# Kernel optimization log

Measured on AMD Instinct MI355X. Metric: run time of the kernel, lower is better.

Reference implementation:

```python
import jax, jax.numpy as jnp
import numpy as np

N = 50000      # num nodes
E = 400000     # directed edges (avg out-degree 8)
DIN = 128
DOUT = 128
ALPHA = 0.5    # args.alphaDir (buffer, requires_grad=False)
BETA = 0.5     # args.betaDir
GAMA = 0.5     # args.gamaDir


def _dedupe(rows, cols, vals, n):
    key = rows.astype(np.int64) * n + cols.astype(np.int64)
    uk, inv = np.unique(key, return_inverse=True)
    v = np.bincount(inv, weights=vals, minlength=uk.shape[0])
    return (uk // n).astype(np.int32), (uk % n).astype(np.int32), v.astype(np.float32)


def _dir_norm(r, c, v, n):
    # directed_norm: D_out^{-1/2} A D_in^{-1/2}, inf -> 0
    in_deg = np.bincount(c, weights=v, minlength=n)
    out_deg = np.bincount(r, weights=v, minlength=n)
    in_is = np.zeros(n); m = in_deg > 0; in_is[m] = in_deg[m] ** -0.5
    out_is = np.zeros(n); m = out_deg > 0; out_is[m] = out_deg[m] ** -0.5
    return r, c, (out_is[r] * v * in_is[c]).astype(np.float32)


def _spgemm(rA, cA, vA, rB, cB, vB, n):
    # sparse @ sparse in COO, vectorized numpy
    order = np.argsort(rB, kind='stable')
    rBs, cBs, vBs = rB[order], cB[order], vB[order]
    degB = np.bincount(rBs, minlength=n)
    indptr = np.concatenate(([0], np.cumsum(degB)))
    counts = degB[cA]
    total = int(counts.sum())
    rep = np.repeat(np.arange(len(rA)), counts)
    first = np.cumsum(counts) - counts
    pos = np.arange(total) - np.repeat(first, counts) + np.repeat(indptr[cA], counts)
    rows = rA[rep]
    cols = cBs[pos]
    vals = vA[rep].astype(np.float64) * vBs[pos]
    return _dedupe(rows, cols, vals, n)


def setup_inputs() -> dict:
    rng = np.random.default_rng(0)
    r0 = rng.integers(0, N, E).astype(np.int64)
    c0 = rng.integers(0, N, E).astype(np.int64)
    r, c, v = _dedupe(r0, c0, np.ones(E, np.float32), N)
    a = _dir_norm(r, c, v, N)                 # adj_norm
    at = _dir_norm(c, r, v, N)                # adj_t_norm
    rr, cc, vv = _spgemm(a[0], a[1], a[2], at[0], at[1], at[2], N)
    aat = _dir_norm(rr, cc, vv, N)            # directed_norm(A @ At)
    rr, cc, vv = _spgemm(at[0], at[1], at[2], a[0], a[1], a[2], N)
    ata = _dir_norm(rr, cc, vv, N)            # directed_norm(At @ A)
    rr, cc, vv = _spgemm(a[0], a[1], a[2], a[0], a[1], a[2], N)
    aa = _dir_norm(rr, cc, vv, N)             # directed_norm(A @ A)
    rr, cc, vv = _spgemm(at[0], at[1], at[2], at[0], at[1], at[2], N)
    atat = _dir_norm(rr, cc, vv, N)           # directed_norm(At @ At)

    key = jax.random.key(0)
    ks = jax.random.split(key, 7)
    x = jax.random.normal(ks[0], (N, DIN), dtype=jnp.float32)
    s = 1.0 / np.sqrt(DIN)

    def lin(k):
        k1, k2 = jax.random.split(k)
        w = jax.random.uniform(k1, (DIN, DOUT), jnp.float32, -s, s)
        b = jax.random.uniform(k2, (DOUT,), jnp.float32, -s, s)
        return w, b

    w_sd, b_sd = lin(ks[1]); w_ds, b_ds = lin(ks[2])
    w0, b0 = lin(ks[3]); w1, b1 = lin(ks[4])
    w2, b2 = lin(ks[5]); w3, b3 = lin(ks[6])

    out = {'x': x,
           'w_sd': w_sd, 'b_sd': b_sd, 'w_ds': w_ds, 'b_ds': b_ds,
           'w0': w0, 'b0': b0, 'w1': w1, 'b1': b1,
           'w2': w2, 'b2': b2, 'w3': w3, 'b3': b3}
    for name, t in (('a', a), ('at', at), ('aat', aat), ('ata', ata), ('aa', aa), ('atat', atat)):
        out[name + '_rows'] = jnp.asarray(t[0])
        out[name + '_cols'] = jnp.asarray(t[1])
        out[name + '_vals'] = jnp.asarray(t[2])
    return out


def _spmm(rows, cols, vals, x):
    # (A @ x)[i] = sum_e vals[e] * x[cols[e]] scattered to rows[e]
    return jax.ops.segment_sum(vals[:, None] * x[cols], rows, num_segments=x.shape[0])


def reference(x, a_rows, a_cols, a_vals, at_rows, at_cols, at_vals,
              aat_rows, aat_cols, aat_vals, ata_rows, ata_cols, ata_vals,
              aa_rows, aa_cols, aa_vals, atat_rows, atat_cols, atat_vals,
              w_sd, b_sd, w_ds, b_ds, w0, b0, w1, b1, w2, b2, w3, b3):
    out1 = ALPHA * (_spmm(a_rows, a_cols, a_vals, x) @ w_sd + b_sd) \
         + (1.0 - ALPHA) * (_spmm(at_rows, at_cols, at_vals, x) @ w_ds + b_ds)
    out2 = BETA * (_spmm(aat_rows, aat_cols, aat_vals, x) @ w0 + b0) \
         + (1.0 - BETA) * (_spmm(ata_rows, ata_cols, ata_vals, x) @ w1 + b1)
    out3 = GAMA * (_spmm(aa_rows, aa_cols, aa_vals, x) @ w2 + b2) \
         + (1.0 - GAMA) * (_spmm(atat_rows, atat_cols, atat_vals, x) @ w3 + b3)
    return out1 + out2 + out3
```

## Files before the change

### kernel.cpp

```cpp
#include <hip/hip_runtime.h>
#include <hip/hip_bf16.h>

#define FD 128

typedef __attribute__((ext_vector_type(8))) short bf16x8;
typedef __attribute__((ext_vector_type(4))) float f32x4;

__device__ __forceinline__ float bfu2f(unsigned short u) {
  return __uint_as_float(((unsigned int)u) << 16);
}
__device__ __forceinline__ float b2f(__hip_bfloat16 v) { return __bfloat162float(v); }
__device__ __forceinline__ unsigned int pk2(float lo, float hi) {
  return (unsigned int)__bfloat16_as_ushort(__float2bfloat16(lo)) |
         ((unsigned int)__bfloat16_as_ushort(__float2bfloat16(hi)) << 16);
}

__device__ __forceinline__ float ldf(const void* p, int i, int ff) {
  return ff ? ((const float*)p)[i] : b2f(((const __hip_bfloat16*)p)[i]);
}
__device__ __forceinline__ int ldi(const void* p, int i, int fi) {
  return fi ? (int)((const long long*)p)[i] : ((const int*)p)[i];
}

__global__ void cvtall_k(const void* __restrict__ rows, const void* __restrict__ cols,
                         const void* __restrict__ vals, int nnz, int n,
                         const void* __restrict__ x,
                         int* __restrict__ r32, int* __restrict__ c32,
                         float* __restrict__ vf, int* __restrict__ cntT,
                         int* flags) {
  __shared__ int cnt[2];
  if (threadIdx.x < 2) cnt[threadIdx.x] = 0;
  __syncthreads();
  const unsigned short* xu = (const unsigned short*)x;
  int big = 0;
  for (int i = threadIdx.x; i < 1024; i += 256) {
    int e = (xu[i] >> 7) & 0xFF;
    if (e >= 0x90) big++;
  }
  if (big) atomicAdd(&cnt[0], big);
  const int* ci = (const int*)cols;
  int zeros = 0;
  for (int i = threadIdx.x; i < 128; i += 256)
    if ((i & 1) && ci[i] == 0) zeros++;
  if (zeros) atomicAdd(&cnt[1], zeros);
  __syncthreads();
  int ff = (cnt[0] > 16) ? 1 : 0;
  int fi = (cnt[1] >= 32) ? 1 : 0;
  if (blockIdx.x == 0 && threadIdx.x == 0) {
    flags[0] = ff;
    flags[1] = fi;
  }
  int i = blockIdx.x * 256 + threadIdx.x;
  if (i >= nnz) return;
  int r = ldi(rows, i, fi);
  int c = ldi(cols, i, fi);
  if ((unsigned)r >= (unsigned)n) r = 0;
  if ((unsigned)c >= (unsigned)n) c = 0;
  r32[i] = r;
  c32[i] = c;
  vf[i] = ldf(vals, i, ff);
  atomicAdd(&cntT[c], 1);
}

__global__ void scanAbs_k(const int* __restrict__ cnt, int n, int* bsum,
                          const int* __restrict__ rows, int nnz, int* rpA, int nb) {
  int blk = blockIdx.x;
  if (blk < nb) {
    __shared__ int sh[256];
    int t = threadIdx.x;
    int i = blk * 256 + t;
    sh[t] = (i < n) ? cnt[i] : 0;
    __syncthreads();
    for (int d = 128; d > 0; d >>= 1) {
      if (t < d) sh[t] += sh[t + d];
      __syncthreads();
    }
    if (t == 0) bsum[blk] = sh[0];
  } else {
    int i = (blk - nb) * 256 + threadIdx.x;
    if (i > n) return;
    int lo = 0, hi = nnz;
    while (lo < hi) { int mid = (lo + hi) >> 1; if (rows[mid] < i) lo = mid + 1; else hi = mid; }
    rpA[i] = lo;
  }
}

__global__ void scanB_k(int* bsum, int nb, int* rpTail) {
  __shared__ int sh[256];
  int t = threadIdx.x;
  int v = (t < nb) ? bsum[t] : 0;
  sh[t] = v;
  __syncthreads();
  int val = v;
  for (int d = 1; d < 256; d <<= 1) {
    int add = (t >= d) ? sh[t - d] : 0;
    __syncthreads();
    val += add;
    sh[t] = val;
    __syncthreads();
  }
  if (t < nb) bsum[t] = val - v;
  if (t == 255) *rpTail = val;
}

__global__ void scanC_k(const int* __restrict__ cnt, int n, const int* __restrict__ bsum,
                        int* rp, int* cur) {
  __shared__ int sh[256];
  int t = threadIdx.x;
  int i = blockIdx.x * 256 + t;
  int v = (i < n) ? cnt[i] : 0;
  sh[t] = v;
  __syncthreads();
  int val = v;
  for (int d = 1; d < 256; d <<= 1) {
    int add = (t >= d) ? sh[t - d] : 0;
    __syncthreads();
    val += add;
    sh[t] = val;
    __syncthreads();
  }
  int ex = val - v + bsum[blockIdx.x];
  if (i < n) { rp[i] = ex; cur[i] = ex; }
}

__global__ void scatter_k(const int* __restrict__ r, const int* __restrict__ c,
                          const float* __restrict__ v, int nnz,
                          int* cur, int* tSrc, float* tVal) {
  int i = blockIdx.x * 256 + threadIdx.x;
  if (i >= nnz) return;
  int p = atomicAdd(&cur[c[i]], 1);
  if ((unsigned)p >= (unsigned)nnz) return;
  tSrc[p] = r[i];
  tVal[p] = v[i];
}

__global__ void nodesum_k(const int* __restrict__ rpA, const float* __restrict__ av,
                          const int* __restrict__ rpT, const float* __restrict__ tv,
                          float* __restrict__ u1, float* __restrict__ v1, int n) {
  int i = blockIdx.x * 256 + threadIdx.x;
  if (i >= n) return;
  float su = 0.f;
  int e0 = rpA[i], e1 = rpA[i + 1];
  for (int j = e0; j < e1; ++j) su += av[j];
  u1[i] = su;
  float sv = 0.f;
  int f0 = rpT[i], f1 = rpT[i + 1];
  for (int j = f0; j < f1; ++j) sv += tv[j];
  v1[i] = sv;
}

__global__ void bias_k(const void* a, const void* b, const void* c, const void* d,
                       const void* e, const void* f, float* bias, const int* flags) {
  int ff = flags[0];
  int i = threadIdx.x;
  bias[i] = 0.5f * (ldf(a, i, ff) + ldf(b, i, ff) + ldf(c, i, ff)
                  + ldf(d, i, ff) + ldf(e, i, ff) + ldf(f, i, ff));
}

__global__ void fill_k(unsigned short* o, int n) {
  int i = blockIdx.x * 256 + threadIdx.x;
  if (i < n) o[i] = 0x3E80;
}

struct W6p { const void* w[6]; };
struct B6p { const void* b[6]; };

__global__ void dpp_k(const int* __restrict__ rpA, const int* __restrict__ ci,
                      const float* __restrict__ av,
                      const int* __restrict__ rpT, const int* __restrict__ ti,
                      const float* __restrict__ tv,
                      const float* __restrict__ u1, const float* __restrict__ v1,
                      float* __restrict__ s1, float* __restrict__ s2,
                      float* __restrict__ s3, float* __restrict__ s4, int n,
                      const void* __restrict__ x, unsigned int* __restrict__ xb, int nx,
                      W6p ws, __hip_bfloat16* __restrict__ Wt,
                      B6p bs, float* __restrict__ bias,
                      const int* flags, int nb, int cvtB) {
  int blk = blockIdx.x;
  if (blk < nb) {
    int i = blk * 256 + threadIdx.x;
    if (i >= n) return;
    float a1 = 0.f, a3 = 0.f;
    int s0 = rpA[i], se = rpA[i + 1];
    for (int j = s0; j < se; ++j) {
      int c = ci[j];
      float v = av[j];
      a1 = fmaf(v, v1[c], a1);
      a3 = fmaf(v, u1[c], a3);
    }
    s1[i] = (a1 > 0.f) ? rsqrtf(a1) : 0.f;
    s3[i] = (a3 > 0.f) ? rsqrtf(a3) : 0.f;
    float a2 = 0.f, a4 = 0.f;
    int t0 = rpT[i], t1 = rpT[i + 1];
    for (int j = t0; j < t1; ++j) {
      int r = ti[j];
      float v = tv[j];
      a2 = fmaf(v, u1[r], a2);
      a4 = fmaf(v, v1[r], a4);
    }
    s2[i] = (a2 > 0.f) ? rsqrtf(a2) : 0.f;
    s4[i] = (a4 > 0.f) ? rsqrtf(a4) : 0.f;
    return;
  }
  int ff = flags[0];
  if (blk < nb + cvtB) {
    int i = ((blk - nb) * 256 + threadIdx.x) * 8;
    if (i >= nx) return;
    uint4 o;
    if (ff) {
      float4 p0 = *(const float4*)((const float*)x + i);
      float4 p1 = *(const float4*)((const float*)x + i + 4);
      o.x = pk2(p0.x, p0.y); o.y = pk2(p0.z, p0.w);
      o.z = pk2(p1.x, p1.y); o.w = pk2(p1.z, p1.w);
    } else {
      o = *(const uint4*)((const unsigned short*)x + i);
    }
    *(uint4*)(xb + i / 2) = o;
    return;
  }
  if (blk < nb + cvtB + 384) {
    int e = (blk - nb - cvtB) * 256 + threadIdx.x;
    if (e >= 6 * 16384) return;
    int seg = e >> 14;
    int r = e & 16383;
    int nn = r >> 7;
    int innerB = (r & 127) << 1;
    int kb = innerB ^ ((nn & 7) << 4);
    int k = kb >> 1;
    Wt[e] = __float2bfloat16(ldf(ws.w[seg], k * 128 + nn, ff));
    return;
  }
  int i = threadIdx.x;
  if (i < FD)
    bias[i] = 0.5f * (ldf(bs.b[0], i, ff) + ldf(bs.b[1], i, ff) + ldf(bs.b[2], i, ff)
                    + ldf(bs.b[3], i, ff) + ldf(bs.b[4], i, ff) + ldf(bs.b[5], i, ff));
}

__global__ void epk_k(const int* __restrict__ cA, const float* __restrict__ vA,
                      const float* __restrict__ sA1, const float* __restrict__ sA2,
                      const int* __restrict__ cT, const float* __restrict__ vT,
                      const float* __restrict__ sT1, const float* __restrict__ sT2,
                      float4* __restrict__ ewA, float4* __restrict__ ewT, int nnz) {
  int i = blockIdx.x * 256 + threadIdx.x;
  if (i < nnz) {
    int c = cA[i];
    float v = vA[i];
    ewA[i] = make_float4(v, v * sA1[c], v * sA2[c], 0.f);
  } else if (i < 2 * nnz) {
    int k = i - nnz;
    int c = cT[k];
    float v = vT[k];
    ewT[k] = make_float4(v, v * sT1[c], v * sT2[c], 0.f);
  }
}

struct FHSet {
  const int* rp; const int* ci; const float4* ew;
  unsigned int* ot; unsigned int* oa; unsigned int* ob;
};

__global__ __launch_bounds__(256) void fh3d_k(
    FHSet h0, FHSet h1, const unsigned int* __restrict__ xb, int n, int half) {
  int blk = blockIdx.x;
  bool hiH = blk >= half;
  const int* rp = hiH ? h1.rp : h0.rp;
  const int* ci = hiH ? h1.ci : h0.ci;
  const float4* ew = hiH ? h1.ew : h0.ew;
  unsigned int* ot = hiH ? h1.ot : h0.ot;
  unsigned int* oa = hiH ? h1.oa : h0.oa;
  unsigned int* ob = hiH ? h1.ob : h0.ob;
  int bb = hiH ? blk - half : blk;

  int wave = threadIdx.x >> 6;
  int l = threadIdx.x & 63;
  int r = bb * 4 + wave;
  if (r >= n) return;
  int s = rp[r], e = rp[r + 1];

  float tl = 0.f, th = 0.f, al = 0.f, ah = 0.f, bl = 0.f, bh = 0.f;
  int j = s;
  for (; j + 3 < e; j += 4) {
#pragma unroll
    for (int u = 0; u < 4; ++u) {
      int c = ci[j + u];
      float4 w = ew[j + u];
      unsigned int xu = xb[(size_t)c * 64 + l];
      float lo = __uint_as_float(xu << 16);
      float hi = __uint_as_float(xu & 0xFFFF0000u);
      tl = fmaf(w.x, lo, tl); th = fmaf(w.x, hi, th);
      al = fmaf(w.y, lo, al); ah = fmaf(w.y, hi, ah);
      bl = fmaf(w.z, lo, bl); bh = fmaf(w.z, hi, bh);
    }
  }
  for (; j < e; ++j) {
    int c = ci[j];
    float4 w = ew[j];
    unsigned int xu = xb[(size_t)c * 64 + l];
    float lo = __uint_as_float(xu << 16);
    float hi = __uint_as_float(xu & 0xFFFF0000u);
    tl = fmaf(w.x, lo, tl); th = fmaf(w.x, hi, th);
    al = fmaf(w.y, lo, al); ah = fmaf(w.y, hi, ah);
    bl = fmaf(w.z, lo, bl); bh = fmaf(w.z, hi, bh);
  }
  ot[(size_t)r * 64 + l] = pk2(tl, th);
  oa[(size_t)r * 128 + l] = pk2(al, ah);
  ob[(size_t)r * 128 + l] = pk2(bl, bh);
}

struct SHSet {
  const int* rp; const int* ci; const float* cv;
  const unsigned int* gp;
  unsigned int* ya; unsigned int* yb;
  const float* rsa; const float* rsb;
};

__global__ __launch_bounds__(256) void sh2d_k(SHSet h0, SHSet h1, int n, int half) {
  int blk = blockIdx.x;
  bool hiH = blk >= half;
  const int* rp = hiH ? h1.rp : h0.rp;
  const int* ci = hiH ? h1.ci : h0.ci;
  const float* cv = hiH ? h1.cv : h0.cv;
  const unsigned int* gp = hiH ? h1.gp : h0.gp;
  unsigned int* ya = hiH ? h1.ya : h0.ya;
  unsigned int* yb = hiH ? h1.yb : h0.yb;
  const float* rsa = hiH ? h1.rsa : h0.rsa;
  const float* rsb = hiH ? h1.rsb : h0.rsb;
  int bb = hiH ? blk - half : blk;

  int wave = threadIdx.x >> 6;
  int l = threadIdx.x & 63;
  int lf = l & 31;
  bool hlo = l < 32;
  int r = bb * 4 + wave;
  if (r >= n) return;
  int s = rp[r], e = rp[r + 1];

  float f0 = 0.f, f1 = 0.f, f2 = 0.f, f3 = 0.f;
  int j = s;
  for (; j + 3 < e; j += 4) {
#pragma unroll
    for (int u = 0; u < 4; ++u) {
      int c = ci[j + u];
      float v = cv[j + u];
      uint2 g = *(const uint2*)(gp + (size_t)c * 128 + l * 2);
      f0 = fmaf(v, __uint_as_float(g.x << 16), f0);
      f1 = fmaf(v, __uint_as_float(g.x & 0xFFFF0000u), f1);
      f2 = fmaf(v, __uint_as_float(g.y << 16), f2);
      f3 = fmaf(v, __uint_as_float(g.y & 0xFFFF0000u), f3);
    }
  }
  for (; j < e; ++j) {
    int c = ci[j];
    float v = cv[j];
    uint2 g = *(const uint2*)(gp + (size_t)c * 128 + l * 2);
    f0 = fmaf(v, __uint_as_float(g.x << 16), f0);
    f1 = fmaf(v, __uint_as_float(g.x & 0xFFFF0000u), f1);
    f2 = fmaf(v, __uint_as_float(g.y << 16), f2);
    f3 = fmaf(v, __uint_as_float(g.y & 0xFFFF0000u), f3);
  }
  float rs = hlo ? rsa[r] : rsb[r];
  unsigned int* yp = hlo ? ya : yb;
  uint2 o;
  o.x = pk2(f0 * rs, f1 * rs);
  o.y = pk2(f2 * rs, f3 * rs);
  *(uint2*)(yp + (size_t)r * 64 + lf * 2) = o;
}

struct Y6 { const unsigned short* y[6]; };

__global__ __launch_bounds__(256) void gemm6m3_k(
    Y6 ys, const unsigned short* __restrict__ Wt2, const float* __restrict__ bias,
    void* __restrict__ outp, int M, const int* flags) {
  int ff = flags[0];
  __shared__ __align__(16) unsigned short Bs[16384];
  const int tid = threadIdx.x;
  const int lane = tid & 63;
  const int wave = tid >> 6;
  const int m = lane & 15;
  const int q = lane >> 4;
  const int r0 = blockIdx.x * 128 + wave * 32;
  const int row0 = r0 + m;
  const int row1 = r0 + 16 + m;
  const bool ok0 = row0 < M;
  const bool ok1 = row1 < M;
  const bf16x8 zero8 = {0, 0, 0, 0, 0, 0, 0, 0};

  f32x4 acc0[8], acc1[8];
#pragma unroll
  for (int nt = 0; nt < 8; ++nt) {
    acc0[nt] = (f32x4){0.f, 0.f, 0.f, 0.f};
    acc1[nt] = (f32x4){0.f, 0.f, 0.f, 0.f};
  }

  bf16x8 Bst[8];
#pragma unroll
  for (int c2 = 0; c2 < 8; ++c2)
    Bst[c2] = *(const bf16x8*)(Wt2 + (size_t)(c2 * 256 + tid) * 8);
  bf16x8 Ap0[4], Ap1[4];
#pragma unroll
  for (int kc = 0; kc < 4; ++kc) {
    Ap0[kc] = ok0 ? *(const bf16x8*)(ys.y[0] + (size_t)row0 * FD + kc * 32 + q * 8) : zero8;
    Ap1[kc] = ok1 ? *(const bf16x8*)(ys.y[0] + (size_t)row1 * FD + kc * 32 + q * 8) : zero8;
  }

  const int swz = (m & 7) << 4;

#pragma unroll
  for (int t = 0; t < 6; ++t) {
    __syncthreads();
#pragma unroll
    for (int c2 = 0; c2 < 8; ++c2)
      *(bf16x8*)((char*)Bs + (size_t)(c2 * 256 + tid) * 16) = Bst[c2];
    bf16x8 A0[4], A1[4];
#pragma unroll
    for (int kc = 0; kc < 4; ++kc) { A0[kc] = Ap0[kc]; A1[kc] = Ap1[kc]; }
    if (t < 5) {
#pragma unroll
      for (int c2 = 0; c2 < 8; ++c2)
        Bst[c2] = *(const bf16x8*)(Wt2 + (size_t)(t + 1) * 16384 +
                                   (size_t)(c2 * 256 + tid) * 8);
#pragma unroll
      for (int kc = 0; kc < 4; ++kc) {
        Ap0[kc] = ok0 ? *(const bf16x8*)(ys.y[t + 1] + (size_t)row0 * FD + kc * 32 + q * 8) : zero8;
        Ap1[kc] = ok1 ? *(const bf16x8*)(ys.y[t + 1] + (size_t)row1 * FD + kc * 32 + q * 8) : zero8;
      }
    }
    __syncthreads();
#pragma unroll
    for (int kc = 0; kc < 4; ++kc) {
      const int koff = (kc * 64 + q * 16) ^ swz;
#pragma unroll
      for (int nt = 0; nt < 8; ++nt) {
        const int nrow = nt * 16 + m;
        bf16x8 bfv = *(const bf16x8*)((const char*)Bs + nrow * 256 + koff);
        acc0[nt] = __builtin_amdgcn_mfma_f32_16x16x32_bf16(A0[kc], bfv, acc0[nt], 0, 0, 0);
        acc1[nt] = __builtin_amdgcn_mfma_f32_16x16x32_bf16(A1[kc], bfv, acc1[nt], 0, 0, 0);
      }
    }
  }

#pragma unroll
  for (int nt = 0; nt < 8; ++nt) {
    int col = nt * 16 + m;
    float bv = bias[col];
#pragma unroll
    for (int rg = 0; rg < 4; ++rg) {
      int g0 = r0 + q * 4 + rg;
      if (g0 < M) {
        float v = 0.5f * acc0[nt][rg] + bv;
        if (ff) ((float*)outp)[(size_t)g0 * FD + col] = v;
        else ((unsigned short*)outp)[(size_t)g0 * FD + col] =
            __bfloat16_as_ushort(__float2bfloat16(v));
      }
      int g1 = r0 + 16 + q * 4 + rg;
      if (g1 < M) {
        float v = 0.5f * acc1[nt][rg] + bv;
        if (ff) ((float*)outp)[(size_t)g1 * FD + col] = v;
        else ((unsigned short*)outp)[(size_t)g1 * FD + col] =
            __bfloat16_as_ushort(__float2bfloat16(v));
      }
    }
  }
}

__global__ __launch_bounds__(128) void spmm_k(
    const int* __restrict__ rp, const void* __restrict__ ci, int cif,
    const void* __restrict__ cv, int cvf,
    const void* __restrict__ x, int xf, __hip_bfloat16* __restrict__ y,
    int n, int nnzMax,
    const float* __restrict__ cscale, const float* __restrict__ rscale,
    const int* flags) {
  int ff = flags[0], fi = flags[1];
  int vf = cvf ? 1 : ff;
  int iw = cif ? fi : 0;
  int xw = xf ? ff : 0;
  const int t = threadIdx.x;
  int r0 = blockIdx.x * 4;
  int rend = min(r0 + 4, n);
  for (int r = r0; r < rend; ++r) {
    int s = rp[r], e = rp[r + 1];
    s = max(0, min(s, nnzMax));
    e = max(s, min(e, nnzMax));
    float acc = 0.f;
    for (int j = s; j < e; ++j) {
      int c = ldi(ci, j, iw);
      if ((unsigned)c >= (unsigned)n) c = 0;
      float v = (vf ? ((const float*)cv)[j] : b2f(((const __hip_bfloat16*)cv)[j]));
      if (cscale) v *= cscale[c];
      float xv = xw ? ((const float*)x)[c * FD + t]
                    : b2f(((const __hip_bfloat16*)x)[c * FD + t]);
      acc = fmaf(v, xv, acc);
    }
    if (rscale) acc *= rscale[r];
    y[r * FD + t] = __float2bfloat16(acc);
  }
}

__global__ __launch_bounds__(256) void gemm_k(
    const __hip_bfloat16* __restrict__ Y, const void* __restrict__ W,
    const float* __restrict__ bias, const void* __restrict__ accin,
    void* __restrict__ outp, int M, const int* flags) {
  int ff = flags[0];
  __shared__ __align__(16) float Wl[32 * 128];
  __shared__ __align__(16) float Yl[64 * 36];
  const int t = threadIdx.x;
  const int row0 = blockIdx.x * 64;
  const int c4 = (t & 31) * 4;
  const int r8 = (t >> 5) * 8;
  const int rs = t >> 3;
  const int q = t & 7;
  float acc[8][4];
#pragma unroll
  for (int m = 0; m < 8; ++m)
#pragma unroll
    for (int j = 0; j < 4; ++j) acc[m][j] = 0.f;
  for (int kc = 0; kc < 4; ++kc) {
    if (ff) {
      const float4* Wg4 = (const float4*)((const float*)W + kc * 32 * 128);
#pragma unroll
      for (int i = 0; i < 4; ++i)
        *(float4*)(Wl + (t + i * 256) * 4) = Wg4[t + i * 256];
    } else {
      const ushort4* Wg4 = (const ushort4*)((const unsigned short*)W + kc * 32 * 128);
#pragma unroll
      for (int i = 0; i < 4; ++i) {
        ushort4 u = Wg4[t + i * 256];
        int base = (t + i * 256) * 4;
        Wl[base + 0] = bfu2f(u.x);
        Wl[base + 1] = bfu2f(u.y);
        Wl[base + 2] = bfu2f(u.z);
        Wl[base + 3] = bfu2f(u.w);
      }
    }
#pragma unroll
    for (int i = 0; i < 2; ++i) {
      int rr = rs + i * 32;
      int grow = row0 + rr;
      ushort4 u = make_ushort4(0, 0, 0, 0);
      if (grow < M)
        u = *(const ushort4*)((const unsigned short*)Y + grow * FD + kc * 32 + q * 4);
      float* yd = Yl + rr * 36 + q * 4;
      yd[0] = bfu2f(u.x); yd[1] = bfu2f(u.y); yd[2] = bfu2f(u.z); yd[3] = bfu2f(u.w);
    }
    __syncthreads();
#pragma unroll
    for (int kk = 0; kk < 32; kk += 4) {
      float4 w0 = *(const float4*)(Wl + (kk + 0) * 128 + c4);
      float4 w1 = *(const float4*)(Wl + (kk + 1) * 128 + c4);
      float4 w2 = *(const float4*)(Wl + (kk + 2) * 128 + c4);
      float4 w3 = *(const float4*)(Wl + (kk + 3) * 128 + c4);
#pragma unroll
      for (int m = 0; m < 8; ++m) {
        float4 yv = *(const float4*)(Yl + (r8 + m) * 36 + kk);
        acc[m][0] = fmaf(yv.x, w0.x, acc[m][0]);
        acc[m][1] = fmaf(yv.x, w0.y, acc[m][1]);
        acc[m][2] = fmaf(yv.x, w0.z, acc[m][2]);
        acc[m][3] = fmaf(yv.x, w0.w, acc[m][3]);
        acc[m][0] = fmaf(yv.y, w1.x, acc[m][0]);
        acc[m][1] = fmaf(yv.y, w1.y, acc[m][1]);
        acc[m][2] = fmaf(yv.y, w1.z, acc[m][2]);
        acc[m][3] = fmaf(yv.y, w1.w, acc[m][3]);
        acc[m][0] = fmaf(yv.z, w2.x, acc[m][0]);
        acc[m][1] = fmaf(yv.z, w2.y, acc[m][1]);
        acc[m][2] = fmaf(yv.z, w2.z, acc[m][2]);
        acc[m][3] = fmaf(yv.z, w2.w, acc[m][3]);
        acc[m][0] = fmaf(yv.w, w3.x, acc[m][0]);
        acc[m][1] = fmaf(yv.w, w3.y, acc[m][1]);
        acc[m][2] = fmaf(yv.w, w3.z, acc[m][2]);
        acc[m][3] = fmaf(yv.w, w3.w, acc[m][3]);
      }
    }
    __syncthreads();
  }
  float4 b4 = make_float4(0.f, 0.f, 0.f, 0.f);
  if (bias) b4 = *(const float4*)(bias + c4);
#pragma unroll
  for (int m = 0; m < 8; ++m) {
    int grow = row0 + r8 + m;
    if (grow >= M) continue;
    float4 rv;
    rv.x = 0.5f * acc[m][0] + b4.x;
    rv.y = 0.5f * acc[m][1] + b4.y;
    rv.z = 0.5f * acc[m][2] + b4.z;
    rv.w = 0.5f * acc[m][3] + b4.w;
    if (accin) {
      if (ff) {
        float4 o = *(const float4*)((const float*)accin + grow * FD + c4);
        rv.x += o.x; rv.y += o.y; rv.z += o.z; rv.w += o.w;
      } else {
        ushort4 o = *(const ushort4*)((const unsigned short*)accin + grow * FD + c4);
        rv.x += bfu2f(o.x); rv.y += bfu2f(o.y); rv.z += bfu2f(o.z); rv.w += bfu2f(o.w);
      }
    }
    if (ff) {
      *(float4*)((float*)outp + grow * FD + c4) = rv;
    } else {
      ushort4 so;
      so.x = __bfloat16_as_ushort(__float2bfloat16(rv.x));
      so.y = __bfloat16_as_ushort(__float2bfloat16(rv.y));
      so.z = __bfloat16_as_ushort(__float2bfloat16(rv.z));
      so.w = __bfloat16_as_ushort(__float2bfloat16(rv.w));
      *(ushort4*)((unsigned short*)outp + grow * FD + c4) = so;
    }
  }
}

extern "C" void kernel_launch(void* const* d_in, const int* in_sizes, int n_in,
                              void* d_out, int out_size, void* d_ws, size_t ws_size,
                              hipStream_t stream) {
  const void* x    = d_in[0];
  const void* w_sd = d_in[1];
  const void* b_sd = d_in[2];
  const void* w_ds = d_in[3];
  const void* b_ds = d_in[4];
  const void* w0   = d_in[5];
  const void* b0   = d_in[6];
  const void* w1   = d_in[7];
  const void* b1   = d_in[8];
  const void* w2   = d_in[9];
  const void* b2   = d_in[10];
  const void* w3   = d_in[11];
  const void* b3   = d_in[12];
  const void* a_rows = d_in[13];
  const void* a_cols = d_in[14];
  const void* a_vals = d_in[15];
  const int nnz = in_sizes[13];
  const int N = in_sizes[0] / FD;

  const size_t BUF = ((size_t)N * FD * 2 + 255) & ~(size_t)255;

  auto misc_need = [&](int nbig) -> size_t {
    size_t need = (size_t)nbig * BUF;
    need += ((size_t)10 * N * 4 + 255) & ~(size_t)255;
    need += 512 + 256 + 1024;
    need += (((size_t)(N + 1) * 4 + 255) & ~(size_t)255) * 2;
    need += (((size_t)N * 4 + 255) & ~(size_t)255) * 2;
    need += (((size_t)nnz * 4 + 255) & ~(size_t)255) * 5;
    need += (6 * 16384 * 2 + 255) & ~(size_t)255;
    need += (((size_t)nnz * 16 + 255) & ~(size_t)255) * 2;
    return need;
  };
  size_t needA = misc_need(10);
  size_t needB = misc_need(2);

  int pathA = (ws_size >= needA) ? 1 : 0;
  if (!pathA && ws_size < needB) {
    fill_k<<<(out_size + 255) / 256, 256, 0, stream>>>((unsigned short*)d_out, out_size);
    return;
  }

  int nbig = pathA ? 10 : 2;
  char* p = (char*)d_ws;
  char* bufs[10];
  for (int i = 0; i < 10; ++i) bufs[i] = (i < nbig) ? (p + (size_t)i * BUF) : nullptr;
  char* q = p + (size_t)nbig * BUF;
  auto take = [&](size_t bytes) -> char* {
    char* r = q;
    q += (bytes + 255) & ~(size_t)255;
    return r;
  };
  float* degf  = (float*)take((size_t)10 * N * 4);
  float* biasf = (float*)take(512);
  int*   flags = (int*)take(256);
  int*   bsum  = (int*)take(1024);
  int* rpA  = (int*)take((size_t)(N + 1) * 4);
  int* rpT  = (int*)take((size_t)(N + 1) * 4);
  int* curT = (int*)take((size_t)N * 4);
  int* cntT = (int*)take((size_t)N * 4);
  int* tSrc = (int*)take((size_t)nnz * 4);
  float* tValF = (float*)take((size_t)nnz * 4);
  int* aRow32 = (int*)take((size_t)nnz * 4);
  int* aCol32 = (int*)take((size_t)nnz * 4);
  float* aValF = (float*)take((size_t)nnz * 4);
  __hip_bfloat16* Wt = (__hip_bfloat16*)take(6 * 16384 * 2);
  float4* ewA = (float4*)take((size_t)nnz * 16);
  float4* ewT = (float4*)take((size_t)nnz * 16);

  float* u1 = degf;
  float* v1 = degf + N;
  float* s1 = degf + 6 * N;
  float* s2 = degf + 7 * N;
  float* s3 = degf + 8 * N;
  float* s4 = degf + 9 * N;

  int eb = (nnz + 255) / 256;
  int nb = (N + 255) / 256;
  int nb2 = (N + 256) / 256;

  hipMemsetAsync(cntT, 0, (size_t)N * 4, stream);
  cvtall_k<<<eb, 256, 0, stream>>>(a_rows, a_cols, a_vals, nnz, N, x,
                                   aRow32, aCol32, aValF, cntT, flags);
  scanAbs_k<<<nb + nb2, 256, 0, stream>>>(cntT, N, bsum, aRow32, nnz, rpA, nb);
  scanB_k<<<1, 256, 0, stream>>>(bsum, nb, rpT + N);
  scanC_k<<<nb, 256, 0, stream>>>(cntT, N, bsum, rpT, curT);
  scatter_k<<<eb, 256, 0, stream>>>(aRow32, aCol32, aValF, nnz, curT, tSrc, tValF);
  nodesum_k<<<nb, 256, 0, stream>>>(rpA, aValF, rpT, tValF, u1, v1, N);

  int sg2 = (N + 3) / 4;
  int gg = (N + 63) / 64;
  int gg4 = (N + 127) / 128;

  W6p wargs;
  wargs.w[0] = w_sd; wargs.w[1] = w_ds; wargs.w[2] = w0;
  wargs.w[3] = w1;   wargs.w[4] = w2;   wargs.w[5] = w3;
  B6p bargs;
  bargs.b[0] = b_sd; bargs.b[1] = b_ds; bargs.b[2] = b0;
  bargs.b[3] = b1;   bargs.b[4] = b2;   bargs.b[5] = b3;

  if (pathA) {
    unsigned int* xbu = (unsigned int*)bufs[0];
    int nx = N * FD;
    int cvtB = (nx / 8 + 255) / 256;
    dpp_k<<<nb + cvtB + 384 + 1, 256, 0, stream>>>(
        rpA, aCol32, aValF, rpT, tSrc, tValF, u1, v1, s1, s2, s3, s4, N,
        x, xbu, nx, wargs, Wt, bargs, biasf, flags, nb, cvtB);
    epk_k<<<(2 * nnz + 255) / 256, 256, 0, stream>>>(
        aCol32, aValF, s2, s4, tSrc, tValF, s1, s3, ewA, ewT, nnz);

    unsigned int* t2 = (unsigned int*)bufs[1];
    unsigned int* t1 = (unsigned int*)bufs[2];
    unsigned int* P1 = (unsigned int*)bufs[3];
    unsigned int* P2 = (unsigned int*)bufs[5];
    unsigned int* y3 = (unsigned int*)bufs[7];
    unsigned int* y4 = (unsigned int*)bufs[8];
    unsigned int* y6 = (unsigned int*)bufs[9];
    unsigned int* y5 = (unsigned int*)bufs[0];

    FHSet hT = { rpT, tSrc, ewT, t2, P1, P2 + 64 };
    FHSet hA = { rpA, aCol32, ewA, t1, P2, P1 + 64 };
    fh3d_k<<<2 * sg2, 256, 0, stream>>>(hT, hA, xbu, N, sg2);

    SHSet sA = { rpA, aCol32, aValF, P1, y3, y5, s1, s3 };
    SHSet sT = { rpT, tSrc, tValF, P2, y4, y6, s2, s4 };
    sh2d_k<<<2 * sg2, 256, 0, stream>>>(sA, sT, N, sg2);

    Y6 yargs;
    yargs.y[0] = (const unsigned short*)t1;
    yargs.y[1] = (const unsigned short*)t2;
    yargs.y[2] = (const unsigned short*)y3;
    yargs.y[3] = (const unsigned short*)y4;
    yargs.y[4] = (const unsigned short*)y5;
    yargs.y[5] = (const unsigned short*)y6;
    gemm6m3_k<<<gg4, 256, 0, stream>>>(yargs, (const unsigned short*)Wt, biasf, d_out, N, flags);
  } else {
    dpp_k<<<nb, 256, 0, stream>>>(
        rpA, aCol32, aValF, rpT, tSrc, tValF, u1, v1, s1, s2, s3, s4, N,
        x, (unsigned int*)bufs[0], 0, wargs, Wt, bargs, biasf, flags, nb, 0);
    bias_k<<<1, FD, 0, stream>>>(b_sd, b_ds, b0, b1, b2, b3, biasf, flags);
    __hip_bfloat16* Yb = (__hip_bfloat16*)bufs[0];
    __hip_bfloat16* gb = (__hip_bfloat16*)bufs[1];
    spmm_k<<<sg2, 128, 0, stream>>>(rpA, a_cols, 1, a_vals, 0, x, 1, Yb, N, nnz, nullptr, nullptr, flags);
    gemm_k<<<gg, 256, 0, stream>>>(Yb, w_sd, biasf, nullptr, d_out, N, flags);
    spmm_k<<<sg2, 128, 0, stream>>>(rpT, tSrc, 0, tValF, 1, x, 1, Yb, N, nnz, nullptr, nullptr, flags);
    gemm_k<<<gg, 256, 0, stream>>>(Yb, w_ds, nullptr, d_out, d_out, N, flags);
    spmm_k<<<sg2, 128, 0, stream>>>(rpT, tSrc, 0, tValF, 1, x, 1, gb, N, nnz, s1, nullptr, flags);
    spmm_k<<<sg2, 128, 0, stream>>>(rpA, a_cols, 1, a_vals, 0, gb, 0, Yb, N, nnz, nullptr, s1, flags);
    gemm_k<<<gg, 256, 0, stream>>>(Yb, w0, nullptr, d_out, d_out, N, flags);
    spmm_k<<<sg2, 128, 0, stream>>>(rpA, a_cols, 1, a_vals, 0, x, 1, gb, N, nnz, s2, nullptr, flags);
    spmm_k<<<sg2, 128, 0, stream>>>(rpT, tSrc, 0, tValF, 1, gb, 0, Yb, N, nnz, nullptr, s2, flags);
    gemm_k<<<gg, 256, 0, stream>>>(Yb, w1, nullptr, d_out, d_out, N, flags);
    spmm_k<<<sg2, 128, 0, stream>>>(rpA, a_cols, 1, a_vals, 0, x, 1, gb, N, nnz, s4, nullptr, flags);
    spmm_k<<<sg2, 128, 0, stream>>>(rpA, a_cols, 1, a_vals, 0, gb, 0, Yb, N, nnz, nullptr, s3, flags);
    gemm_k<<<gg, 256, 0, stream>>>(Yb, w2, nullptr, d_out, d_out, N, flags);
    spmm_k<<<sg2, 128, 0, stream>>>(rpT, tSrc, 0, tValF, 1, x, 1, gb, N, nnz, s3, nullptr, flags);
    spmm_k<<<sg2, 128, 0, stream>>>(rpT, tSrc, 0, tValF, 1, gb, 0, Yb, N, nnz, nullptr, s4, flags);
    gemm_k<<<gg, 256, 0, stream>>>(Yb, w3, nullptr, d_out, d_out, N, flags);
  }
}
```

Before: 440.9 us.

## Pack column index and value into int2 pairs, merge scan kernels, unroll gathers

```diff
diff --git a/kernel.cpp b/kernel.cpp
--- a/kernel.cpp
+++ b/kernel.cpp
@@ -25,9 +25,8 @@
 __global__ void cvtall_k(const void* __restrict__ rows, const void* __restrict__ cols,
                          const void* __restrict__ vals, int nnz, int n,
                          const void* __restrict__ x,
-                         int* __restrict__ r32, int* __restrict__ c32,
-                         float* __restrict__ vf, int* __restrict__ cntT,
-                         int* flags) {
+                         int* __restrict__ r32, int2* __restrict__ aP,
+                         int* __restrict__ cntT, int* flags) {
   __shared__ int cnt[2];
   if (threadIdx.x < 2) cnt[threadIdx.x] = 0;
   __syncthreads();
@@ -57,8 +56,7 @@
   if ((unsigned)r >= (unsigned)n) r = 0;
   if ((unsigned)c >= (unsigned)n) c = 0;
   r32[i] = r;
-  c32[i] = c;
-  vf[i] = ldf(vals, i, ff);
+  aP[i] = make_int2(c, __float_as_int(ldf(vals, i, ff)));
   atomicAdd(&cntT[c], 1);
 }
 
@@ -85,28 +83,17 @@
   }
 }
 
-__global__ void scanB_k(int* bsum, int nb, int* rpTail) {
+__global__ void scanC_k(const int* __restrict__ cnt, int n, const int* __restrict__ bsum,
+                        int* rp, int* cur, int nnz) {
   __shared__ int sh[256];
+  __shared__ int base;
   int t = threadIdx.x;
-  int v = (t < nb) ? bsum[t] : 0;
-  sh[t] = v;
-  __syncthreads();
-  int val = v;
-  for (int d = 1; d < 256; d <<= 1) {
-    int add = (t >= d) ? sh[t - d] : 0;
-    __syncthreads();
-    val += add;
-    sh[t] = val;
-    __syncthreads();
-  }
-  if (t < nb) bsum[t] = val - v;
-  if (t == 255) *rpTail = val;
-}
-
-__global__ void scanC_k(const int* __restrict__ cnt, int n, const int* __restrict__ bsum,
-                        int* rp, int* cur) {
-  __shared__ int sh[256];
-  int t = threadIdx.x;
+  if (t == 0) {
+    int s = 0;
+    for (int b = 0; b < blockIdx.x; ++b) s += bsum[b];
+    base = s;
+    if (blockIdx.x == 0) rp[n] = nnz;
+  }
   int i = blockIdx.x * 256 + t;
   int v = (i < n) ? cnt[i] : 0;
   sh[t] = v;
@@ -119,33 +106,32 @@
     sh[t] = val;
     __syncthreads();
   }
-  int ex = val - v + bsum[blockIdx.x];
+  int ex = val - v + base;
   if (i < n) { rp[i] = ex; cur[i] = ex; }
 }
 
-__global__ void scatter_k(const int* __restrict__ r, const int* __restrict__ c,
-                          const float* __restrict__ v, int nnz,
-                          int* cur, int* tSrc, float* tVal) {
+__global__ void scatter_k(const int* __restrict__ r, const int2* __restrict__ aP,
+                          int nnz, int* cur, int2* __restrict__ tP) {
   int i = blockIdx.x * 256 + threadIdx.x;
   if (i >= nnz) return;
-  int p = atomicAdd(&cur[c[i]], 1);
+  int2 pr = aP[i];
+  int p = atomicAdd(&cur[pr.x], 1);
   if ((unsigned)p >= (unsigned)nnz) return;
-  tSrc[p] = r[i];
-  tVal[p] = v[i];
-}
-
-__global__ void nodesum_k(const int* __restrict__ rpA, const float* __restrict__ av,
-                          const int* __restrict__ rpT, const float* __restrict__ tv,
+  tP[p] = make_int2(r[i], pr.y);
+}
+
+__global__ void nodesum_k(const int* __restrict__ rpA, const int2* __restrict__ aP,
+                          const int* __restrict__ rpT, const int2* __restrict__ tP,
                           float* __restrict__ u1, float* __restrict__ v1, int n) {
   int i = blockIdx.x * 256 + threadIdx.x;
   if (i >= n) return;
   float su = 0.f;
   int e0 = rpA[i], e1 = rpA[i + 1];
-  for (int j = e0; j < e1; ++j) su += av[j];
+  for (int j = e0; j < e1; ++j) su += __int_as_float(aP[j].y);
   u1[i] = su;
   float sv = 0.f;
   int f0 = rpT[i], f1 = rpT[i + 1];
-  for (int j = f0; j < f1; ++j) sv += tv[j];
+  for (int j = f0; j < f1; ++j) sv += __int_as_float(tP[j].y);
   v1[i] = sv;
 }
 
@@ -165,10 +151,8 @@
 struct W6p { const void* w[6]; };
 struct B6p { const void* b[6]; };
 
-__global__ void dpp_k(const int* __restrict__ rpA, const int* __restrict__ ci,
-                      const float* __restrict__ av,
-                      const int* __restrict__ rpT, const int* __restrict__ ti,
-                      const float* __restrict__ tv,
+__global__ void dpp_k(const int* __restrict__ rpA, const int2* __restrict__ aP,
+                      const int* __restrict__ rpT, const int2* __restrict__ tP,
                       const float* __restrict__ u1, const float* __restrict__ v1,
                       float* __restrict__ s1, float* __restrict__ s2,
                       float* __restrict__ s3, float* __restrict__ s4, int n,
@@ -183,20 +167,20 @@
     float a1 = 0.f, a3 = 0.f;
     int s0 = rpA[i], se = rpA[i + 1];
     for (int j = s0; j < se; ++j) {
-      int c = ci[j];
-      float v = av[j];
-      a1 = fmaf(v, v1[c], a1);
-      a3 = fmaf(v, u1[c], a3);
+      int2 pr = aP[j];
+      float v = __int_as_float(pr.y);
+      a1 = fmaf(v, v1[pr.x], a1);
+      a3 = fmaf(v, u1[pr.x], a3);
     }
     s1[i] = (a1 > 0.f) ? rsqrtf(a1) : 0.f;
     s3[i] = (a3 > 0.f) ? rsqrtf(a3) : 0.f;
     float a2 = 0.f, a4 = 0.f;
     int t0 = rpT[i], t1 = rpT[i + 1];
     for (int j = t0; j < t1; ++j) {
-      int r = ti[j];
-      float v = tv[j];
-      a2 = fmaf(v, u1[r], a2);
-      a4 = fmaf(v, v1[r], a4);
+      int2 pr = tP[j];
+      float v = __int_as_float(pr.y);
+      a2 = fmaf(v, u1[pr.x], a2);
+      a4 = fmaf(v, v1[pr.x], a4);
     }
     s2[i] = (a2 > 0.f) ? rsqrtf(a2) : 0.f;
     s4[i] = (a4 > 0.f) ? rsqrtf(a4) : 0.f;
@@ -236,35 +220,49 @@
                     + ldf(bs.b[3], i, ff) + ldf(bs.b[4], i, ff) + ldf(bs.b[5], i, ff));
 }
 
-__global__ void epk_k(const int* __restrict__ cA, const float* __restrict__ vA,
+__global__ void epk_k(const int2* __restrict__ pA,
                       const float* __restrict__ sA1, const float* __restrict__ sA2,
-                      const int* __restrict__ cT, const float* __restrict__ vT,
+                      const int2* __restrict__ pT,
                       const float* __restrict__ sT1, const float* __restrict__ sT2,
                       float4* __restrict__ ewA, float4* __restrict__ ewT, int nnz) {
   int i = blockIdx.x * 256 + threadIdx.x;
   if (i < nnz) {
-    int c = cA[i];
-    float v = vA[i];
-    ewA[i] = make_float4(v, v * sA1[c], v * sA2[c], 0.f);
+    int2 pr = pA[i];
+    float v = __int_as_float(pr.y);
+    ewA[i] = make_float4(v, v * sA1[pr.x], v * sA2[pr.x], 0.f);
   } else if (i < 2 * nnz) {
     int k = i - nnz;
-    int c = cT[k];
-    float v = vT[k];
-    ewT[k] = make_float4(v, v * sT1[c], v * sT2[c], 0.f);
+    int2 pr = pT[k];
+    float v = __int_as_float(pr.y);
+    ewT[k] = make_float4(v, v * sT1[pr.x], v * sT2[pr.x], 0.f);
   }
 }
 
 struct FHSet {
-  const int* rp; const int* ci; const float4* ew;
+  const int* rp; const int2* pr; const float4* ew;
   unsigned int* ot; unsigned int* oa; unsigned int* ob;
 };
+
+__device__ __forceinline__ void fh_step(const int2* pr, const float4* ew, int j,
+                                        const unsigned int* xb, int l,
+                                        float& tl, float& th, float& al, float& ah,
+                                        float& bl, float& bh) {
+  int c = pr[j].x;
+  float4 w = ew[j];
+  unsigned int xu = xb[(size_t)c * 64 + l];
+  float lo = __uint_as_float(xu << 16);
+  float hi = __uint_as_float(xu & 0xFFFF0000u);
+  tl = fmaf(w.x, lo, tl); th = fmaf(w.x, hi, th);
+  al = fmaf(w.y, lo, al); ah = fmaf(w.y, hi, ah);
+  bl = fmaf(w.z, lo, bl); bh = fmaf(w.z, hi, bh);
+}
 
 __global__ __launch_bounds__(256) void fh3d_k(
     FHSet h0, FHSet h1, const unsigned int* __restrict__ xb, int n, int half) {
   int blk = blockIdx.x;
   bool hiH = blk >= half;
   const int* rp = hiH ? h1.rp : h0.rp;
-  const int* ci = hiH ? h1.ci : h0.ci;
+  const int2* pr = hiH ? h1.pr : h0.pr;
   const float4* ew = hiH ? h1.ew : h0.ew;
   unsigned int* ot = hiH ? h1.ot : h0.ot;
   unsigned int* oa = hiH ? h1.oa : h0.oa;
@@ -279,47 +277,48 @@
 
   float tl = 0.f, th = 0.f, al = 0.f, ah = 0.f, bl = 0.f, bh = 0.f;
   int j = s;
+  for (; j + 7 < e; j += 8) {
+#pragma unroll
+    for (int u = 0; u < 8; ++u)
+      fh_step(pr, ew, j + u, xb, l, tl, th, al, ah, bl, bh);
+  }
   for (; j + 3 < e; j += 4) {
 #pragma unroll
-    for (int u = 0; u < 4; ++u) {
-      int c = ci[j + u];
-      float4 w = ew[j + u];
-      unsigned int xu = xb[(size_t)c * 64 + l];
-      float lo = __uint_as_float(xu << 16);
-      float hi = __uint_as_float(xu & 0xFFFF0000u);
-      tl = fmaf(w.x, lo, tl); th = fmaf(w.x, hi, th);
-      al = fmaf(w.y, lo, al); ah = fmaf(w.y, hi, ah);
-      bl = fmaf(w.z, lo, bl); bh = fmaf(w.z, hi, bh);
-    }
-  }
-  for (; j < e; ++j) {
-    int c = ci[j];
-    float4 w = ew[j];
-    unsigned int xu = xb[(size_t)c * 64 + l];
-    float lo = __uint_as_float(xu << 16);
-    float hi = __uint_as_float(xu & 0xFFFF0000u);
-    tl = fmaf(w.x, lo, tl); th = fmaf(w.x, hi, th);
-    al = fmaf(w.y, lo, al); ah = fmaf(w.y, hi, ah);
-    bl = fmaf(w.z, lo, bl); bh = fmaf(w.z, hi, bh);
-  }
+    for (int u = 0; u < 4; ++u)
+      fh_step(pr, ew, j + u, xb, l, tl, th, al, ah, bl, bh);
+  }
+  for (; j < e; ++j)
+    fh_step(pr, ew, j, xb, l, tl, th, al, ah, bl, bh);
+
   ot[(size_t)r * 64 + l] = pk2(tl, th);
   oa[(size_t)r * 128 + l] = pk2(al, ah);
   ob[(size_t)r * 128 + l] = pk2(bl, bh);
 }
 
 struct SHSet {
-  const int* rp; const int* ci; const float* cv;
+  const int* rp; const int2* pr;
   const unsigned int* gp;
   unsigned int* ya; unsigned int* yb;
   const float* rsa; const float* rsb;
 };
 
+__device__ __forceinline__ void sh_step(const int2* pr, int j,
+                                        const unsigned int* gp, int l,
+                                        float& f0, float& f1, float& f2, float& f3) {
+  int2 p = pr[j];
+  float v = __int_as_float(p.y);
+  uint2 g = *(const uint2*)(gp + (size_t)p.x * 128 + l * 2);
+  f0 = fmaf(v, __uint_as_float(g.x << 16), f0);
+  f1 = fmaf(v, __uint_as_float(g.x & 0xFFFF0000u), f1);
+  f2 = fmaf(v, __uint_as_float(g.y << 16), f2);
+  f3 = fmaf(v, __uint_as_float(g.y & 0xFFFF0000u), f3);
+}
+
 __global__ __launch_bounds__(256) void sh2d_k(SHSet h0, SHSet h1, int n, int half) {
   int blk = blockIdx.x;
   bool hiH = blk >= half;
   const int* rp = hiH ? h1.rp : h0.rp;
-  const int* ci = hiH ? h1.ci : h0.ci;
-  const float* cv = hiH ? h1.cv : h0.cv;
+  const int2* pr = hiH ? h1.pr : h0.pr;
   const unsigned int* gp = hiH ? h1.gp : h0.gp;
   unsigned int* ya = hiH ? h1.ya : h0.ya;
   unsigned int* yb = hiH ? h1.yb : h0.yb;
@@ -337,27 +336,19 @@
 
   float f0 = 0.f, f1 = 0.f, f2 = 0.f, f3 = 0.f;
   int j = s;
+  for (; j + 7 < e; j += 8) {
+#pragma unroll
+    for (int u = 0; u < 8; ++u)
+      sh_step(pr, j + u, gp, l, f0, f1, f2, f3);
+  }
   for (; j + 3 < e; j += 4) {
 #pragma unroll
-    for (int u = 0; u < 4; ++u) {
-      int c = ci[j + u];
-      float v = cv[j + u];
-      uint2 g = *(const uint2*)(gp + (size_t)c * 128 + l * 2);
-      f0 = fmaf(v, __uint_as_float(g.x << 16), f0);
-      f1 = fmaf(v, __uint_as_float(g.x & 0xFFFF0000u), f1);
-      f2 = fmaf(v, __uint_as_float(g.y << 16), f2);
-      f3 = fmaf(v, __uint_as_float(g.y & 0xFFFF0000u), f3);
-    }
-  }
-  for (; j < e; ++j) {
-    int c = ci[j];
-    float v = cv[j];
-    uint2 g = *(const uint2*)(gp + (size_t)c * 128 + l * 2);
-    f0 = fmaf(v, __uint_as_float(g.x << 16), f0);
-    f1 = fmaf(v, __uint_as_float(g.x & 0xFFFF0000u), f1);
-    f2 = fmaf(v, __uint_as_float(g.y << 16), f2);
-    f3 = fmaf(v, __uint_as_float(g.y & 0xFFFF0000u), f3);
-  }
+    for (int u = 0; u < 4; ++u)
+      sh_step(pr, j + u, gp, l, f0, f1, f2, f3);
+  }
+  for (; j < e; ++j)
+    sh_step(pr, j, gp, l, f0, f1, f2, f3);
+
   float rs = hlo ? rsa[r] : rsb[r];
   unsigned int* yp = hlo ? ya : yb;
   uint2 o;
@@ -471,8 +462,6 @@
     const float* __restrict__ cscale, const float* __restrict__ rscale,
     const int* flags) {
   int ff = flags[0], fi = flags[1];
-  int vf = cvf ? 1 : ff;
-  int iw = cif ? fi : 0;
   int xw = xf ? ff : 0;
   const int t = threadIdx.x;
   int r0 = blockIdx.x * 4;
@@ -483,9 +472,17 @@
     e = max(s, min(e, nnzMax));
     float acc = 0.f;
     for (int j = s; j < e; ++j) {
-      int c = ldi(ci, j, iw);
+      int c;
+      float v;
+      if (cif == 2) {
+        int2 pr = ((const int2*)ci)[j];
+        c = pr.x;
+        v = __int_as_float(pr.y);
+      } else {
+        c = ldi(ci, j, fi);
+        v = (cvf ? ((const float*)cv)[j] : ldf(cv, j, ff));
+      }
       if ((unsigned)c >= (unsigned)n) c = 0;
-      float v = (vf ? ((const float*)cv)[j] : b2f(((const __hip_bfloat16*)cv)[j]));
       if (cscale) v *= cscale[c];
       float xv = xw ? ((const float*)x)[c * FD + t]
                     : b2f(((const __hip_bfloat16*)x)[c * FD + t]);
@@ -635,7 +632,8 @@
     need += 512 + 256 + 1024;
     need += (((size_t)(N + 1) * 4 + 255) & ~(size_t)255) * 2;
     need += (((size_t)N * 4 + 255) & ~(size_t)255) * 2;
-    need += (((size_t)nnz * 4 + 255) & ~(size_t)255) * 5;
+    need += ((size_t)nnz * 4 + 255) & ~(size_t)255;
+    need += (((size_t)nnz * 8 + 255) & ~(size_t)255) * 2;
     need += (6 * 16384 * 2 + 255) & ~(size_t)255;
     need += (((size_t)nnz * 16 + 255) & ~(size_t)255) * 2;
     return need;
@@ -667,11 +665,9 @@
   int* rpT  = (int*)take((size_t)(N + 1) * 4);
   int* curT = (int*)take((size_t)N * 4);
   int* cntT = (int*)take((size_t)N * 4);
-  int* tSrc = (int*)take((size_t)nnz * 4);
-  float* tValF = (float*)take((size_t)nnz * 4);
   int* aRow32 = (int*)take((size_t)nnz * 4);
-  int* aCol32 = (int*)take((size_t)nnz * 4);
-  float* aValF = (float*)take((size_t)nnz * 4);
+  int2* aPair = (int2*)take((size_t)nnz * 8);
+  int2* tPair = (int2*)take((size_t)nnz * 8);
   __hip_bfloat16* Wt = (__hip_bfloat16*)take(6 * 16384 * 2);
   float4* ewA = (float4*)take((size_t)nnz * 16);
   float4* ewT = (float4*)take((size_t)nnz * 16);
@@ -689,12 +685,11 @@
 
   hipMemsetAsync(cntT, 0, (size_t)N * 4, stream);
   cvtall_k<<<eb, 256, 0, stream>>>(a_rows, a_cols, a_vals, nnz, N, x,
-                                   aRow32, aCol32, aValF, cntT, flags);
+                                   aRow32, aPair, cntT, flags);
   scanAbs_k<<<nb + nb2, 256, 0, stream>>>(cntT, N, bsum, aRow32, nnz, rpA, nb);
-  scanB_k<<<1, 256, 0, stream>>>(bsum, nb, rpT + N);
-  scanC_k<<<nb, 256, 0, stream>>>(cntT, N, bsum, rpT, curT);
-  scatter_k<<<eb, 256, 0, stream>>>(aRow32, aCol32, aValF, nnz, curT, tSrc, tValF);
-  nodesum_k<<<nb, 256, 0, stream>>>(rpA, aValF, rpT, tValF, u1, v1, N);
+  scanC_k<<<nb, 256, 0, stream>>>(cntT, N, bsum, rpT, curT, nnz);
+  scatter_k<<<eb, 256, 0, stream>>>(aRow32, aPair, nnz, curT, tPair);
+  nodesum_k<<<nb, 256, 0, stream>>>(rpA, aPair, rpT, tPair, u1, v1, N);
 
   int sg2 = (N + 3) / 4;
   int gg = (N + 63) / 64;
@@ -712,10 +707,10 @@
     int nx = N * FD;
     int cvtB = (nx / 8 + 255) / 256;
     dpp_k<<<nb + cvtB + 384 + 1, 256, 0, stream>>>(
-        rpA, aCol32, aValF, rpT, tSrc, tValF, u1, v1, s1, s2, s3, s4, N,
+        rpA, aPair, rpT, tPair, u1, v1, s1, s2, s3, s4, N,
         x, xbu, nx, wargs, Wt, bargs, biasf, flags, nb, cvtB);
     epk_k<<<(2 * nnz + 255) / 256, 256, 0, stream>>>(
-        aCol32, aValF, s2, s4, tSrc, tValF, s1, s3, ewA, ewT, nnz);
+        aPair, s2, s4, tPair, s1, s3, ewA, ewT, nnz);
 
     unsigned int* t2 = (unsigned int*)bufs[1];
     unsigned int* t1 = (unsigned int*)bufs[2];
@@ -726,12 +721,12 @@
     unsigned int* y6 = (unsigned int*)bufs[9];
     unsigned int* y5 = (unsigned int*)bufs[0];
 
-    FHSet hT = { rpT, tSrc, ewT, t2, P1, P2 + 64 };
-    FHSet hA = { rpA, aCol32, ewA, t1, P2, P1 + 64 };
+    FHSet hT = { rpT, tPair, ewT, t2, P1, P2 + 64 };
+    FHSet hA = { rpA, aPair, ewA, t1, P2, P1 + 64 };
     fh3d_k<<<2 * sg2, 256, 0, stream>>>(hT, hA, xbu, N, sg2);
 
-    SHSet sA = { rpA, aCol32, aValF, P1, y3, y5, s1, s3 };
-    SHSet sT = { rpT, tSrc, tValF, P2, y4, y6, s2, s4 };
+    SHSet sA = { rpA, aPair, P1, y3, y5, s1, s3 };
+    SHSet sT = { rpT, tPair, P2, y4, y6, s2, s4 };
     sh2d_k<<<2 * sg2, 256, 0, stream>>>(sA, sT, N, sg2);
 
     Y6 yargs;
@@ -744,26 +739,26 @@
     gemm6m3_k<<<gg4, 256, 0, stream>>>(yargs, (const unsigned short*)Wt, biasf, d_out, N, flags);
   } else {
     dpp_k<<<nb, 256, 0, stream>>>(
-        rpA, aCol32, aValF, rpT, tSrc, tValF, u1, v1, s1, s2, s3, s4, N,
+        rpA, aPair, rpT, tPair, u1, v1, s1, s2, s3, s4, N,
         x, (unsigned int*)bufs[0], 0, wargs, Wt, bargs, biasf, flags, nb, 0);
     bias_k<<<1, FD, 0, stream>>>(b_sd, b_ds, b0, b1, b2, b3, biasf, flags);
     __hip_bfloat16* Yb = (__hip_bfloat16*)bufs[0];
     __hip_bfloat16* gb = (__hip_bfloat16*)bufs[1];
     spmm_k<<<sg2, 128, 0, stream>>>(rpA, a_cols, 1, a_vals, 0, x, 1, Yb, N, nnz, nullptr, nullptr, flags);
     gemm_k<<<gg, 256, 0, stream>>>(Yb, w_sd, biasf, nullptr, d_out, N, flags);
-    spmm_k<<<sg2, 128, 0, stream>>>(rpT, tSrc, 0, tValF, 1, x, 1, Yb, N, nnz, nullptr, nullptr, flags);
+    spmm_k<<<sg2, 128, 0, stream>>>(rpT, tPair, 2, nullptr, 0, x, 1, Yb, N, nnz, nullptr, nullptr, flags);
     gemm_k<<<gg, 256, 0, stream>>>(Yb, w_ds, nullptr, d_out, d_out, N, flags);
-    spmm_k<<<sg2, 128, 0, stream>>>(rpT, tSrc, 0, tValF, 1, x, 1, gb, N, nnz, s1, nullptr, flags);
+    spmm_k<<<sg2, 128, 0, stream>>>(rpT, tPair, 2, nullptr, 0, x, 1, gb, N, nnz, s1, nullptr, flags);
     spmm_k<<<sg2, 128, 0, stream>>>(rpA, a_cols, 1, a_vals, 0, gb, 0, Yb, N, nnz, nullptr, s1, flags);
     gemm_k<<<gg, 256, 0, stream>>>(Yb, w0, nullptr, d_out, d_out, N, flags);
     spmm_k<<<sg2, 128, 0, stream>>>(rpA, a_cols, 1, a_vals, 0, x, 1, gb, N, nnz, s2, nullptr, flags);
-    spmm_k<<<sg2, 128, 0, stream>>>(rpT, tSrc, 0, tValF, 1, gb, 0, Yb, N, nnz, nullptr, s2, flags);
+    spmm_k<<<sg2, 128, 0, stream>>>(rpT, tPair, 2, nullptr, 0, gb, 0, Yb, N, nnz, nullptr, s2, flags);
     gemm_k<<<gg, 256, 0, stream>>>(Yb, w1, nullptr, d_out, d_out, N, flags);
     spmm_k<<<sg2, 128, 0, stream>>>(rpA, a_cols, 1, a_vals, 0, x, 1, gb, N, nnz, s4, nullptr, flags);
     spmm_k<<<sg2, 128, 0, stream>>>(rpA, a_cols, 1, a_vals, 0, gb, 0, Yb, N, nnz, nullptr, s3, flags);
     gemm_k<<<gg, 256, 0, stream>>>(Yb, w2, nullptr, d_out, d_out, N, flags);
-    spmm_k<<<sg2, 128, 0, stream>>>(rpT, tSrc, 0, tValF, 1, x, 1, gb, N, nnz, s3, nullptr, flags);
-    spmm_k<<<sg2, 128, 0, stream>>>(rpT, tSrc, 0, tValF, 1, gb, 0, Yb, N, nnz, nullptr, s4, flags);
+    spmm_k<<<sg2, 128, 0, stream>>>(rpT, tPair, 2, nullptr, 0, x, 1, gb, N, nnz, s3, nullptr, flags);
+    spmm_k<<<sg2, 128, 0, stream>>>(rpT, tPair, 2, nullptr, 0, gb, 0, Yb, N, nnz, nullptr, s4, flags);
     gemm_k<<<gg, 256, 0, stream>>>(Yb, w3, nullptr, d_out, d_out, N, flags);
   }
 }
```

Measured after the change: 443.0 us. Within noise of the previous version (+0.5%).
